# Performance work log

Measured on AMD Instinct MI355X. Metric: run time of the kernel, lower is better.

Reference implementation:

```python
import jax, jax.numpy as jnp
import numpy as np


def setup_inputs() -> dict:
    key = jax.random.key(0)
    ks = jax.random.split(key, 5)
    B, C, H, W = 4, 256, 48, 48
    x = jax.random.normal(ks[0], (B, C, H, W), dtype=jnp.float32)
    w_qkv = jax.random.normal(ks[1], (3 * C, C), dtype=jnp.float32) * (C ** -0.5)
    b_qkv = jax.random.normal(ks[2], (3 * C,), dtype=jnp.float32) * 0.02
    w_proj = jax.random.normal(ks[3], (C, C), dtype=jnp.float32) * (C ** -0.5)
    b_proj = jax.random.normal(ks[4], (C,), dtype=jnp.float32) * 0.02
    return {"x": x, "w_qkv": w_qkv, "b_qkv": b_qkv, "w_proj": w_proj, "b_proj": b_proj, "num_heads": 4}


def reference(x, w_qkv, b_qkv, w_proj, b_proj, num_heads):
    B, C, H, W = x.shape
    N = H * W
    hd = C // num_heads
    # NOTE: original uses full-dim scale, not head_dim
    scale = C ** -0.5
    # 1x1 conv == channel matmul
    qkv = jnp.einsum('bchw,oc->bohw', x, w_qkv) + b_qkv[None, :, None, None]
    qkv = qkv.reshape(B, 3, num_heads, hd, N)
    q = qkv[:, 0].transpose(0, 1, 3, 2)  # [B, h, N, d]
    k = qkv[:, 1]                         # [B, h, d, N]
    v = qkv[:, 2].transpose(0, 1, 3, 2)  # [B, h, N, d]
    attn = jax.nn.softmax((q @ k) * scale, axis=-1)  # [B, h, N, N]
    out = attn @ v                        # [B, h, N, d]
    out = out.transpose(0, 1, 3, 2).reshape(B, C, H, W)
    return jnp.einsum('bchw,oc->bohw', out, w_proj) + b_proj[None, :, None, None]
```

## Files before the change

kernel.cpp:

```cpp
#include <hip/hip_runtime.h>
#include <hip/hip_bf16.h>
#include <stdint.h>

typedef unsigned short u16;
typedef unsigned int u32;
typedef __attribute__((ext_vector_type(8))) short bf16x8;
typedef __attribute__((ext_vector_type(4))) float f32x4;
typedef __attribute__((ext_vector_type(4))) unsigned short u16x4;

#define MFMA16 __builtin_amdgcn_mfma_f32_16x16x32_bf16

static constexpr int Bb = 4;
static constexpr int Cc = 256;
static constexpr int NHh = 4;
static constexpr int HDd = 64;
static constexpr int Nn = 2304;

__device__ __forceinline__ u16 f2bf(float f) {
  u32 u = __builtin_bit_cast(u32, f);
  u32 r = u + 0x7fffu + ((u >> 16) & 1u);
  return (u16)(r >> 16);
}

__device__ __forceinline__ u32 pkbf(float a, float b) {
  return (u32)f2bf(a) | ((u32)f2bf(b) << 16);
}

__device__ __forceinline__ u32 cvtpk(float a, float b) {
  u32 r;
  asm("v_cvt_pk_bf16_f32 %0, %1, %2" : "=v"(r) : "v"(a), "v"(b));
  return r;
}

__device__ __forceinline__ float blo(u32 u) { return __builtin_bit_cast(float, u << 16); }
__device__ __forceinline__ float bhi(u32 u) { return __builtin_bit_cast(float, u & 0xffff0000u); }

__device__ __forceinline__ void async16(const void* g, void* l) {
  __builtin_amdgcn_global_load_lds(
      (const __attribute__((address_space(1))) u32*)g,
      (__attribute__((address_space(3))) u32*)l, 16, 0, 0);
}

__global__ void k_cast_w(const float* __restrict__ wq, const float* __restrict__ wp,
                         u16* __restrict__ wqb, u16* __restrict__ wpb) {
  int i = blockIdx.x * 256 + threadIdx.x;
  if (i < 3 * Cc * Cc) wqb[i] = f2bf(wq[i]);
  if (i < Cc * Cc)     wpb[i] = f2bf(wp[i]);
}

__global__ __launch_bounds__(256) void k_transpose_x(const float* __restrict__ x,
                                                     u16* __restrict__ xT) {
  __shared__ float tile[64][65];
  int c0 = blockIdx.x * 64, n0 = blockIdx.y * 64, b = blockIdx.z;
  int w = threadIdx.x >> 6, lane = threadIdx.x & 63;
#pragma unroll
  for (int i = 0; i < 16; ++i) {
    int c = i * 4 + w;
    tile[c][lane] = x[((size_t)(b * Cc + c0 + c)) * Nn + n0 + lane];
  }
  __syncthreads();
#pragma unroll
  for (int i = 0; i < 16; ++i) {
    int n = i * 4 + w;
    xT[((size_t)(b * Nn + n0 + n)) * Cc + c0 + lane] = f2bf(tile[lane][n]);
  }
}

__global__ __launch_bounds__(256) void k_qkv(const u16* __restrict__ wqb,
                                             const u16* __restrict__ xT,
                                             const float* __restrict__ bqkv,
                                             u16* __restrict__ qT, u16* __restrict__ kT,
                                             u16* __restrict__ vT) {
  __shared__ u16 Bs[64 * 256];
  int o0 = blockIdx.x * 64, n0 = blockIdx.y * 64, b = blockIdx.z;
  int t = threadIdx.x, w = t >> 6, l = t & 63, g = l >> 4, li = l & 15;
#pragma unroll
  for (int it = 0; it < 8; ++it) {
    int ch = it * 256 + t;
    int row = ch >> 5, c16 = ch & 31;
    const char* src = (const char*)xT + ((size_t)(b * Nn + n0 + row)) * 512 +
                      ((c16 * 16) ^ ((row & 7) << 4));
    async16(src, (char*)Bs + (it * 256 + (t & ~63)) * 16);
  }
  const u16* Arow = wqb + (size_t)(o0 + w * 16 + li) * Cc;
  __syncthreads();
  f32x4 acc[4] = {};
#pragma unroll
  for (int s = 0; s < 8; ++s) {
    bf16x8 a = *(const bf16x8*)(Arow + s * 32 + g * 8);
#pragma unroll
    for (int nt = 0; nt < 4; ++nt) {
      int row = nt * 16 + li;
      const char* bp_ = (const char*)Bs + row * 512 + ((s * 64 + g * 16) ^ ((row & 7) << 4));
      bf16x8 bb = *(const bf16x8*)bp_;
      acc[nt] = MFMA16(a, bb, acc[nt], 0, 0, 0);
    }
  }
  int which = o0 >> 8;
  int hh = (o0 >> 6) & 3;
  int bh = b * NHh + hh;
  int dbase = w * 16 + g * 4;
  const float qs = 0.0625f * 1.44269504088896340736f;
#pragma unroll
  for (int nt = 0; nt < 4; ++nt) {
    int n = n0 + nt * 16 + li;
    float v0 = acc[nt][0] + bqkv[o0 + dbase + 0];
    float v1 = acc[nt][1] + bqkv[o0 + dbase + 1];
    float v2 = acc[nt][2] + bqkv[o0 + dbase + 2];
    float v3 = acc[nt][3] + bqkv[o0 + dbase + 3];
    if (which == 0) {
      u16x4 p = {f2bf(v0 * qs), f2bf(v1 * qs), f2bf(v2 * qs), f2bf(v3 * qs)};
      *(u16x4*)(qT + ((size_t)bh * Nn + n) * HDd + dbase) = p;
    } else if (which == 1) {
      u16x4 p = {f2bf(v0), f2bf(v1), f2bf(v2), f2bf(v3)};
      *(u16x4*)(kT + ((size_t)bh * Nn + n) * HDd + dbase) = p;
    } else {
      vT[((size_t)bh * HDd + dbase + 0) * Nn + n] = f2bf(v0);
      vT[((size_t)bh * HDd + dbase + 1) * Nn + n] = f2bf(v1);
      vT[((size_t)bh * HDd + dbase + 2) * Nn + n] = f2bf(v2);
      vT[((size_t)bh * HDd + dbase + 3) * Nn + n] = f2bf(v3);
    }
  }
}

__global__ __launch_bounds__(192) void k_attn(const u16* __restrict__ qT,
                                              const u16* __restrict__ kT,
                                              const u16* __restrict__ vT,
                                              u16* __restrict__ attP,
                                              float* __restrict__ lsumP) {
  __shared__ u16 Ks[2][32 * 64];
  __shared__ u16 Vs[2][64 * 32];
  __shared__ u16 Ps[3][16 * 64];
  int L = blockIdx.x;
  int xcd = L & 7, r = L >> 3;
  int bh = 2 * xcd + (r >= 96 ? 1 : 0);
  int rr = (r >= 96) ? r - 96 : r;
  int half = (rr >= 48) ? 1 : 0;
  int qb = (rr >= 48) ? rr - 48 : rr;
  int t = threadIdx.x, w = t / 64, l = t & 63, g = l >> 4, li = l & 15;
  int q0 = qb * 48 + w * 16;
  const u16* qrow = qT + ((size_t)bh * Nn + q0 + li) * HDd;
  bf16x8 bq0 = *(const bf16x8*)(qrow + g * 8);
  bf16x8 bq1 = *(const bf16x8*)(qrow + 32 + g * 8);
  const short one = (short)0x3F80;
  bf16x8 ONES = {one, one, one, one, one, one, one, one};
  f32x4 acc[4] = {};
  f32x4 acc_l = {};
  const char* kbh = (const char*)(kT + (size_t)bh * Nn * HDd);
  const char* vbh = (const char*)(vT + (size_t)bh * HDd * Nn);
  char* PsB = (char*)(&Ps[w][0]);
  int sw_li = (li & 7) << 4;
  int sw_v  = (li & 3) << 4;

  const char* sp[3];
  int sd[3], sstr[3];
  bool son[3], svv[3];
#pragma unroll
  for (int it = 0; it < 3; ++it) {
    int gg = w * 3 + it;
    son[it] = (gg < 8);
    int c = gg * 64 + l;
    if (c < 256) {
      int key = c >> 3, c8 = c & 7;
      sp[it] = kbh + (size_t)(half * 1152 + key) * 128 + ((c8 * 16) ^ ((key & 7) << 4));
      sd[it] = c * 16; sstr[it] = 32 * 128; svv[it] = false;
    } else {
      int cv = c - 256, d = cv >> 2, c4 = cv & 3;
      sp[it] = vbh + (size_t)d * (Nn * 2) + half * 2304 + ((c4 * 16) ^ ((d & 3) << 4));
      sd[it] = cv * 16; sstr[it] = 32 * 2; svv[it] = true;
    }
  }

  auto STAGE = [&](int buf) {
    char* kdst = (char*)(&Ks[0][0]) + buf * 4096;
    char* vdst = (char*)(&Vs[0][0]) + buf * 4096;
#pragma unroll
    for (int it = 0; it < 3; ++it) {
      if (son[it]) {
        async16(sp[it], (svv[it] ? vdst : kdst) + sd[it]);
        sp[it] += sstr[it];
      }
    }
  };

  STAGE(0);
  int cur = 0;
  for (int kb = 0; kb < 36; ++kb) {
    __syncthreads();
    if (kb + 1 < 36) STAGE(cur ^ 1);

    const char* Kc = (const char*)(&Ks[0][0]) + cur * 4096;
    const char* Vc = (const char*)(&Vs[0][0]) + cur * 4096;

    f32x4 s[2];
    __builtin_amdgcn_s_setprio(1);
#pragma unroll
    for (int kt = 0; kt < 2; ++kt) {
      const char* kr = Kc + (kt * 16 + li) * 128;
      bf16x8 a0 = *(const bf16x8*)(kr + ((g * 16) ^ sw_li));
      bf16x8 a1 = *(const bf16x8*)(kr + ((64 + g * 16) ^ sw_li));
      f32x4 z = {};
      z = MFMA16(a0, bq0, z, 0, 0, 0);
      z = MFMA16(a1, bq1, z, 0, 0, 0);
      s[kt] = z;
    }
    __builtin_amdgcn_s_setprio(0);

#pragma unroll
    for (int kt = 0; kt < 2; ++kt)
#pragma unroll
      for (int rr2 = 0; rr2 < 4; ++rr2) s[kt][rr2] = exp2f(s[kt][rr2]);

#pragma unroll
    for (int kt = 0; kt < 2; ++kt) {
      uint2 pk;
      pk.x = cvtpk(s[kt][0], s[kt][1]);
      pk.y = cvtpk(s[kt][2], s[kt][3]);
      *(uint2*)(PsB + li * 128 + ((kt * 32 + g * 8) ^ sw_li)) = pk;
    }
    bf16x8 pa0 = *(const bf16x8*)(PsB + li * 128 + ((g * 16) ^ sw_li));
    __builtin_amdgcn_s_setprio(1);
    acc_l = MFMA16(pa0, ONES, acc_l, 0, 0, 0);
#pragma unroll
    for (int dt = 0; dt < 4; ++dt) {
      const char* vr = Vc + (dt * 16 + li) * 64;
      bf16x8 v0 = *(const bf16x8*)(vr + ((g * 16) ^ sw_v));
      acc[dt] = MFMA16(pa0, v0, acc[dt], 0, 0, 0);
    }
    __builtin_amdgcn_s_setprio(0);
    cur ^= 1;
  }
  u16* ap = attP + (size_t)half * (Bb * Nn * Cc);
  float* lp = lsumP + half * (4 * NHh * Nn);
  if (li == 0) {
#pragma unroll
    for (int rr2 = 0; rr2 < 4; ++rr2) lp[bh * Nn + q0 + g * 4 + rr2] = acc_l[rr2];
  }
  int b = bh >> 2, hh = bh & 3;
#pragma unroll
  for (int dt = 0; dt < 4; ++dt) {
    int cidx = hh * 64 + dt * 16 + li;
#pragma unroll
    for (int rr2 = 0; rr2 < 4; ++rr2) {
      ap[((size_t)(b * Nn + q0 + g * 4 + rr2)) * Cc + cidx] = f2bf(acc[dt][rr2]);
    }
  }
}

__global__ __launch_bounds__(256) void k_norm(const u16* __restrict__ attP,
                                              const float* __restrict__ lsumP,
                                              u16* __restrict__ attT) {
  int gid = blockIdx.x * 256 + threadIdx.x;
  int base = gid * 8;
  int bidx = base / (Nn * Cc);
  int rem = base - bidx * (Nn * Cc);
  int n = rem >> 8, c = rem & 255;
  int hh = c >> 6;
  int lidx = (bidx * NHh + hh) * Nn + n;
  float inv = 1.0f / (lsumP[lidx] + lsumP[4 * NHh * Nn + lidx]);
  uint4 p0 = *(const uint4*)(attP + base);
  uint4 p1 = *(const uint4*)(attP + (size_t)(Bb * Nn * Cc) + base);
  uint4 o;
  o.x = pkbf((blo(p0.x) + blo(p1.x)) * inv, (bhi(p0.x) + bhi(p1.x)) * inv);
  o.y = pkbf((blo(p0.y) + blo(p1.y)) * inv, (bhi(p0.y) + bhi(p1.y)) * inv);
  o.z = pkbf((blo(p0.z) + blo(p1.z)) * inv, (bhi(p0.z) + bhi(p1.z)) * inv);
  o.w = pkbf((blo(p0.w) + blo(p1.w)) * inv, (bhi(p0.w) + bhi(p1.w)) * inv);
  *(uint4*)(attT + base) = o;
}

__global__ __launch_bounds__(256) void k_proj(const u16* __restrict__ wpb,
                                              const u16* __restrict__ attT,
                                              const float* __restrict__ bp,
                                              float* __restrict__ out) {
  __shared__ u16 Bs[64 * 256];
  int o0 = blockIdx.x * 64, n0 = blockIdx.y * 64, b = blockIdx.z;
  int t = threadIdx.x, w = t >> 6, l = t & 63, g = l >> 4, li = l & 15;
#pragma unroll
  for (int it = 0; it < 8; ++it) {
    int ch = it * 256 + t;
    int row = ch >> 5, c16 = ch & 31;
    const char* src = (const char*)attT + ((size_t)(b * Nn + n0 + row)) * 512 +
                      ((c16 * 16) ^ ((row & 7) << 4));
    async16(src, (char*)Bs + (it * 256 + (t & ~63)) * 16);
  }
  const u16* Arow = wpb + (size_t)(o0 + w * 16 + li) * Cc;
  __syncthreads();
  f32x4 acc[4] = {};
#pragma unroll
  for (int s = 0; s < 8; ++s) {
    bf16x8 a = *(const bf16x8*)(Arow + s * 32 + g * 8);
#pragma unroll
    for (int nt = 0; nt < 4; ++nt) {
      int row = nt * 16 + li;
      const char* bp_ = (const char*)Bs + row * 512 + ((s * 64 + g * 16) ^ ((row & 7) << 4));
      bf16x8 bb = *(const bf16x8*)bp_;
      acc[nt] = MFMA16(a, bb, acc[nt], 0, 0, 0);
    }
  }
  int obase = o0 + w * 16 + g * 4;
#pragma unroll
  for (int nt = 0; nt < 4; ++nt) {
    int n = n0 + nt * 16 + li;
    out[((size_t)(b * Cc + obase + 0)) * Nn + n] = acc[nt][0] + bp[obase + 0];
    out[((size_t)(b * Cc + obase + 1)) * Nn + n] = acc[nt][1] + bp[obase + 1];
    out[((size_t)(b * Cc + obase + 2)) * Nn + n] = acc[nt][2] + bp[obase + 2];
    out[((size_t)(b * Cc + obase + 3)) * Nn + n] = acc[nt][3] + bp[obase + 3];
  }
}

extern "C" void kernel_launch(void* const* d_in, const int* in_sizes, int n_in,
                              void* d_out, int out_size, void* d_ws, size_t ws_size,
                              hipStream_t stream) {
  const float* x     = (const float*)d_in[0];
  const float* wqkv  = (const float*)d_in[1];
  const float* bqkv  = (const float*)d_in[2];
  const float* wproj = (const float*)d_in[3];
  const float* bproj = (const float*)d_in[4];
  float* out = (float*)d_out;

  u16* ws    = (u16*)d_ws;
  u16* wq_bf = ws;
  u16* wp_bf = wq_bf + 196608;
  u16* xT    = wp_bf + 65536;
  u16* qT    = xT + 2359296;
  u16* kT    = qT + 2359296;
  u16* vT    = kT + 2359296;
  u16* attT  = vT + 2359296;
  u16* attP  = attT + 2359296;
  float* lsumP = (float*)(attP + 2 * 2359296);

  k_cast_w<<<dim3(768), dim3(256), 0, stream>>>(wqkv, wproj, wq_bf, wp_bf);
  k_transpose_x<<<dim3(4, 36, 4), dim3(256), 0, stream>>>(x, xT);
  k_qkv<<<dim3(12, 36, 4), dim3(256), 0, stream>>>(wq_bf, xT, bqkv, qT, kT, vT);
  k_attn<<<dim3(1536), dim3(192), 0, stream>>>(qT, kT, vT, attP, lsumP);
  k_norm<<<dim3(1152), dim3(256), 0, stream>>>(attP, lsumP, attT);
  k_proj<<<dim3(4, 36, 4), dim3(256), 0, stream>>>(wp_bf, attT, bproj, out);
}
```

Measured before the change: 87.17 us.

## Fuse split-K normalization into projection GEMM and merge prep kernels

Drops the separate normalization kernel. The projection now loads both partial attention outputs directly and does the sum over the K-split as extra MFMA work. Each head's partial product goes into its own accumulator, and the per-head 1/l scaling is applied in the epilogue. The weight-cast and transpose kernels are merged into one launch, and each QKV block now computes two output tiles so the staged x tile is reused. The goal is to cut launch overhead and the extra round trip of the attention output through global memory, at the cost of double the MFMA work in proj and smaller n-tiles there.

```diff
diff --git a/kernel.cpp b/kernel.cpp
--- a/kernel.cpp
+++ b/kernel.cpp
@@ -22,36 +22,34 @@
   return (u16)(r >> 16);
 }
 
-__device__ __forceinline__ u32 pkbf(float a, float b) {
-  return (u32)f2bf(a) | ((u32)f2bf(b) << 16);
-}
-
 __device__ __forceinline__ u32 cvtpk(float a, float b) {
   u32 r;
   asm("v_cvt_pk_bf16_f32 %0, %1, %2" : "=v"(r) : "v"(a), "v"(b));
   return r;
 }
 
-__device__ __forceinline__ float blo(u32 u) { return __builtin_bit_cast(float, u << 16); }
-__device__ __forceinline__ float bhi(u32 u) { return __builtin_bit_cast(float, u & 0xffff0000u); }
-
 __device__ __forceinline__ void async16(const void* g, void* l) {
   __builtin_amdgcn_global_load_lds(
       (const __attribute__((address_space(1))) u32*)g,
       (__attribute__((address_space(3))) u32*)l, 16, 0, 0);
 }
 
-__global__ void k_cast_w(const float* __restrict__ wq, const float* __restrict__ wp,
-                         u16* __restrict__ wqb, u16* __restrict__ wpb) {
-  int i = blockIdx.x * 256 + threadIdx.x;
-  if (i < 3 * Cc * Cc) wqb[i] = f2bf(wq[i]);
-  if (i < Cc * Cc)     wpb[i] = f2bf(wp[i]);
-}
-
-__global__ __launch_bounds__(256) void k_transpose_x(const float* __restrict__ x,
-                                                     u16* __restrict__ xT) {
+__global__ __launch_bounds__(256) void k_prep(const float* __restrict__ wq,
+                                              const float* __restrict__ wp,
+                                              const float* __restrict__ x,
+                                              u16* __restrict__ wqb,
+                                              u16* __restrict__ wpb,
+                                              u16* __restrict__ xT) {
   __shared__ float tile[64][65];
-  int c0 = blockIdx.x * 64, n0 = blockIdx.y * 64, b = blockIdx.z;
+  int bx = blockIdx.x;
+  if (bx < 768) {
+    int i = bx * 256 + threadIdx.x;
+    if (i < 3 * Cc * Cc) wqb[i] = f2bf(wq[i]);
+    if (i < Cc * Cc)     wpb[i] = f2bf(wp[i]);
+    return;
+  }
+  int t2 = bx - 768;
+  int c0 = (t2 & 3) * 64, n0 = ((t2 >> 2) % 36) * 64, b = (t2 >> 2) / 36;
   int w = threadIdx.x >> 6, lane = threadIdx.x & 63;
 #pragma unroll
   for (int i = 0; i < 16; ++i) {
@@ -72,7 +70,7 @@
                                              u16* __restrict__ qT, u16* __restrict__ kT,
                                              u16* __restrict__ vT) {
   __shared__ u16 Bs[64 * 256];
-  int o0 = blockIdx.x * 64, n0 = blockIdx.y * 64, b = blockIdx.z;
+  int n0 = blockIdx.y * 64, b = blockIdx.z;
   int t = threadIdx.x, w = t >> 6, l = t & 63, g = l >> 4, li = l & 15;
 #pragma unroll
   for (int it = 0; it < 8; ++it) {
@@ -82,43 +80,47 @@
                       ((c16 * 16) ^ ((row & 7) << 4));
     async16(src, (char*)Bs + (it * 256 + (t & ~63)) * 16);
   }
-  const u16* Arow = wqb + (size_t)(o0 + w * 16 + li) * Cc;
   __syncthreads();
-  f32x4 acc[4] = {};
-#pragma unroll
-  for (int s = 0; s < 8; ++s) {
-    bf16x8 a = *(const bf16x8*)(Arow + s * 32 + g * 8);
+  const float qs = 0.0625f * 1.44269504088896340736f;
+#pragma unroll
+  for (int p = 0; p < 2; ++p) {
+    int o0 = blockIdx.x * 128 + p * 64;
+    const u16* Arow = wqb + (size_t)(o0 + w * 16 + li) * Cc;
+    f32x4 acc[4] = {};
+#pragma unroll
+    for (int s = 0; s < 8; ++s) {
+      bf16x8 a = *(const bf16x8*)(Arow + s * 32 + g * 8);
+#pragma unroll
+      for (int nt = 0; nt < 4; ++nt) {
+        int row = nt * 16 + li;
+        const char* bp_ = (const char*)Bs + row * 512 + ((s * 64 + g * 16) ^ ((row & 7) << 4));
+        bf16x8 bb = *(const bf16x8*)bp_;
+        acc[nt] = MFMA16(a, bb, acc[nt], 0, 0, 0);
+      }
+    }
+    int which = o0 >> 8;
+    int hh = (o0 >> 6) & 3;
+    int bh = b * NHh + hh;
+    int dbase = w * 16 + g * 4;
 #pragma unroll
     for (int nt = 0; nt < 4; ++nt) {
-      int row = nt * 16 + li;
-      const char* bp_ = (const char*)Bs + row * 512 + ((s * 64 + g * 16) ^ ((row & 7) << 4));
-      bf16x8 bb = *(const bf16x8*)bp_;
-      acc[nt] = MFMA16(a, bb, acc[nt], 0, 0, 0);
-    }
-  }
-  int which = o0 >> 8;
-  int hh = (o0 >> 6) & 3;
-  int bh = b * NHh + hh;
-  int dbase = w * 16 + g * 4;
-  const float qs = 0.0625f * 1.44269504088896340736f;
-#pragma unroll
-  for (int nt = 0; nt < 4; ++nt) {
-    int n = n0 + nt * 16 + li;
-    float v0 = acc[nt][0] + bqkv[o0 + dbase + 0];
-    float v1 = acc[nt][1] + bqkv[o0 + dbase + 1];
-    float v2 = acc[nt][2] + bqkv[o0 + dbase + 2];
-    float v3 = acc[nt][3] + bqkv[o0 + dbase + 3];
-    if (which == 0) {
-      u16x4 p = {f2bf(v0 * qs), f2bf(v1 * qs), f2bf(v2 * qs), f2bf(v3 * qs)};
-      *(u16x4*)(qT + ((size_t)bh * Nn + n) * HDd + dbase) = p;
-    } else if (which == 1) {
-      u16x4 p = {f2bf(v0), f2bf(v1), f2bf(v2), f2bf(v3)};
-      *(u16x4*)(kT + ((size_t)bh * Nn + n) * HDd + dbase) = p;
-    } else {
-      vT[((size_t)bh * HDd + dbase + 0) * Nn + n] = f2bf(v0);
-      vT[((size_t)bh * HDd + dbase + 1) * Nn + n] = f2bf(v1);
-      vT[((size_t)bh * HDd + dbase + 2) * Nn + n] = f2bf(v2);
-      vT[((size_t)bh * HDd + dbase + 3) * Nn + n] = f2bf(v3);
+      int n = n0 + nt * 16 + li;
+      float v0 = acc[nt][0] + bqkv[o0 + dbase + 0];
+      float v1 = acc[nt][1] + bqkv[o0 + dbase + 1];
+      float v2 = acc[nt][2] + bqkv[o0 + dbase + 2];
+      float v3 = acc[nt][3] + bqkv[o0 + dbase + 3];
+      if (which == 0) {
+        u16x4 pq = {f2bf(v0 * qs), f2bf(v1 * qs), f2bf(v2 * qs), f2bf(v3 * qs)};
+        *(u16x4*)(qT + ((size_t)bh * Nn + n) * HDd + dbase) = pq;
+      } else if (which == 1) {
+        u16x4 pk = {f2bf(v0), f2bf(v1), f2bf(v2), f2bf(v3)};
+        *(u16x4*)(kT + ((size_t)bh * Nn + n) * HDd + dbase) = pk;
+      } else {
+        vT[((size_t)bh * HDd + dbase + 0) * Nn + n] = f2bf(v0);
+        vT[((size_t)bh * HDd + dbase + 1) * Nn + n] = f2bf(v1);
+        vT[((size_t)bh * HDd + dbase + 2) * Nn + n] = f2bf(v2);
+        vT[((size_t)bh * HDd + dbase + 3) * Nn + n] = f2bf(v3);
+      }
     }
   }
 }
@@ -231,7 +233,7 @@
     cur ^= 1;
   }
   u16* ap = attP + (size_t)half * (Bb * Nn * Cc);
-  float* lp = lsumP + half * (4 * NHh * Nn);
+  float* lp = lsumP + half * (Bb * NHh * Nn);
   if (li == 0) {
 #pragma unroll
     for (int rr2 = 0; rr2 < 4; ++rr2) lp[bh * Nn + q0 + g * 4 + rr2] = acc_l[rr2];
@@ -247,64 +249,58 @@
   }
 }
 
-__global__ __launch_bounds__(256) void k_norm(const u16* __restrict__ attP,
+__global__ __launch_bounds__(256) void k_proj(const u16* __restrict__ wpb,
+                                              const u16* __restrict__ attP,
                                               const float* __restrict__ lsumP,
-                                              u16* __restrict__ attT) {
-  int gid = blockIdx.x * 256 + threadIdx.x;
-  int base = gid * 8;
-  int bidx = base / (Nn * Cc);
-  int rem = base - bidx * (Nn * Cc);
-  int n = rem >> 8, c = rem & 255;
-  int hh = c >> 6;
-  int lidx = (bidx * NHh + hh) * Nn + n;
-  float inv = 1.0f / (lsumP[lidx] + lsumP[4 * NHh * Nn + lidx]);
-  uint4 p0 = *(const uint4*)(attP + base);
-  uint4 p1 = *(const uint4*)(attP + (size_t)(Bb * Nn * Cc) + base);
-  uint4 o;
-  o.x = pkbf((blo(p0.x) + blo(p1.x)) * inv, (bhi(p0.x) + bhi(p1.x)) * inv);
-  o.y = pkbf((blo(p0.y) + blo(p1.y)) * inv, (bhi(p0.y) + bhi(p1.y)) * inv);
-  o.z = pkbf((blo(p0.z) + blo(p1.z)) * inv, (bhi(p0.z) + bhi(p1.z)) * inv);
-  o.w = pkbf((blo(p0.w) + blo(p1.w)) * inv, (bhi(p0.w) + bhi(p1.w)) * inv);
-  *(uint4*)(attT + base) = o;
-}
-
-__global__ __launch_bounds__(256) void k_proj(const u16* __restrict__ wpb,
-                                              const u16* __restrict__ attT,
                                               const float* __restrict__ bp,
                                               float* __restrict__ out) {
-  __shared__ u16 Bs[64 * 256];
-  int o0 = blockIdx.x * 64, n0 = blockIdx.y * 64, b = blockIdx.z;
+  __shared__ u16 Bs[2][32 * 256];
+  int o0 = blockIdx.x * 64, n0 = blockIdx.y * 32, b = blockIdx.z;
   int t = threadIdx.x, w = t >> 6, l = t & 63, g = l >> 4, li = l & 15;
 #pragma unroll
   for (int it = 0; it < 8; ++it) {
     int ch = it * 256 + t;
-    int row = ch >> 5, c16 = ch & 31;
-    const char* src = (const char*)attT + ((size_t)(b * Nn + n0 + row)) * 512 +
+    int hf = ch >> 10, rem = ch & 1023;
+    int row = rem >> 5, c16 = rem & 31;
+    const char* src = (const char*)(attP + (size_t)hf * (Bb * Nn * Cc)) +
+                      ((size_t)(b * Nn + n0 + row)) * 512 +
                       ((c16 * 16) ^ ((row & 7) << 4));
     async16(src, (char*)Bs + (it * 256 + (t & ~63)) * 16);
   }
   const u16* Arow = wpb + (size_t)(o0 + w * 16 + li) * Cc;
   __syncthreads();
-  f32x4 acc[4] = {};
+  f32x4 acc[4][2] = {};
 #pragma unroll
   for (int s = 0; s < 8; ++s) {
     bf16x8 a = *(const bf16x8*)(Arow + s * 32 + g * 8);
 #pragma unroll
-    for (int nt = 0; nt < 4; ++nt) {
-      int row = nt * 16 + li;
-      const char* bp_ = (const char*)Bs + row * 512 + ((s * 64 + g * 16) ^ ((row & 7) << 4));
-      bf16x8 bb = *(const bf16x8*)bp_;
-      acc[nt] = MFMA16(a, bb, acc[nt], 0, 0, 0);
+    for (int hf = 0; hf < 2; ++hf) {
+#pragma unroll
+      for (int nt = 0; nt < 2; ++nt) {
+        int row = nt * 16 + li;
+        const char* bp_ = (const char*)Bs + hf * (32 * 512) + row * 512 +
+                          ((s * 64 + g * 16) ^ ((row & 7) << 4));
+        bf16x8 bb = *(const bf16x8*)bp_;
+        acc[s >> 1][nt] = MFMA16(a, bb, acc[s >> 1][nt], 0, 0, 0);
+      }
     }
   }
   int obase = o0 + w * 16 + g * 4;
 #pragma unroll
-  for (int nt = 0; nt < 4; ++nt) {
+  for (int nt = 0; nt < 2; ++nt) {
     int n = n0 + nt * 16 + li;
-    out[((size_t)(b * Cc + obase + 0)) * Nn + n] = acc[nt][0] + bp[obase + 0];
-    out[((size_t)(b * Cc + obase + 1)) * Nn + n] = acc[nt][1] + bp[obase + 1];
-    out[((size_t)(b * Cc + obase + 2)) * Nn + n] = acc[nt][2] + bp[obase + 2];
-    out[((size_t)(b * Cc + obase + 3)) * Nn + n] = acc[nt][3] + bp[obase + 3];
+    float inv[4];
+#pragma unroll
+    for (int h = 0; h < 4; ++h) {
+      int lidx = (b * NHh + h) * Nn + n;
+      inv[h] = 1.0f / (lsumP[lidx] + lsumP[Bb * NHh * Nn + lidx]);
+    }
+#pragma unroll
+    for (int rr2 = 0; rr2 < 4; ++rr2) {
+      float v = acc[0][nt][rr2] * inv[0] + acc[1][nt][rr2] * inv[1] +
+                acc[2][nt][rr2] * inv[2] + acc[3][nt][rr2] * inv[3];
+      out[((size_t)(b * Cc + obase + rr2)) * Nn + n] = v + bp[obase + rr2];
+    }
   }
 }
 
@@ -325,14 +321,11 @@
   u16* qT    = xT + 2359296;
   u16* kT    = qT + 2359296;
   u16* vT    = kT + 2359296;
-  u16* attT  = vT + 2359296;
-  u16* attP  = attT + 2359296;
+  u16* attP  = vT + 2359296;
   float* lsumP = (float*)(attP + 2 * 2359296);
 
-  k_cast_w<<<dim3(768), dim3(256), 0, stream>>>(wqkv, wproj, wq_bf, wp_bf);
-  k_transpose_x<<<dim3(4, 36, 4), dim3(256), 0, stream>>>(x, xT);
-  k_qkv<<<dim3(12, 36, 4), dim3(256), 0, stream>>>(wq_bf, xT, bqkv, qT, kT, vT);
+  k_prep<<<dim3(1344), dim3(256), 0, stream>>>(wqkv, wproj, x, wq_bf, wp_bf, xT);
+  k_qkv<<<dim3(6, 36, 4), dim3(256), 0, stream>>>(wq_bf, xT, bqkv, qT, kT, vT);
   k_attn<<<dim3(1536), dim3(192), 0, stream>>>(qT, kT, vT, attP, lsumP);
-  k_norm<<<dim3(1152), dim3(256), 0, stream>>>(attP, lsumP, attT);
-  k_proj<<<dim3(4, 36, 4), dim3(256), 0, stream>>>(wp_bf, attT, bproj, out);
-}
+  k_proj<<<dim3(4, 72, 4), dim3(256), 0, stream>>>(wp_bf, attP, lsumP, bproj, out);
+}
```

Result: faster. 84.60 us (-3.0%).
